# Performance work log

Hardware: AMD Instinct MI355X
Metric: run time of the kernel (lower is better)

The kernel has to match this reference:

```python
import jax, jax.numpy as jnp
import numpy as np

N_CLASSES = 16384
M = 2
D = 128


def setup_inputs() -> dict:
    key = jax.random.key(0)
    k1, k2 = jax.random.split(key)
    x = jax.random.normal(k1, (N_CLASSES * M, D), dtype=jnp.float32)
    anchor_idx = jax.random.randint(k2, (N_CLASSES,), 0, M, dtype=jnp.int64 if jax.config.jax_enable_x64 else jnp.int32).astype(jnp.int32)
    pos_idx = (1 - anchor_idx).astype(jnp.int32)  # randperm(2) -> positive is the other sample
    return {"x": x, "anchor_idx": anchor_idx, "pos_idx": pos_idx}


def reference(x, anchor_idx, pos_idx):
    # x: [N*M, D]; anchor_idx/pos_idx: [N] in [0, M)
    N = anchor_idx.shape[0]
    Dx = x.shape[1]
    xr = x.reshape(N, M, Dx)
    anchors = jnp.take_along_axis(xr, anchor_idx[:, None, None], axis=1)[:, 0, :]    # [N, D]
    positives = jnp.take_along_axis(xr, pos_idx[:, None, None], axis=1)[:, 0, :]     # [N, D]
    negs = xr[:, 1, :]                                                               # [N, D] (sample 1 of every class)
    # score[i, j] = a_i . (neg_j - pos_i) = a_i . neg_j - a_i . pos_i
    S = anchors @ negs.T                                                             # [N, N]
    ap = jnp.sum(anchors * positives, axis=1)                                        # [N]
    logits = S - ap[:, None]
    mask = ~jnp.eye(N, dtype=bool)                                                   # exclude j == i (own class)
    sums = jnp.sum(jnp.where(mask, jnp.exp(logits), jnp.float32(0.0)), axis=1)       # [N]
    return jnp.sum(jnp.log1p(sums))
```

## Files before the change

kernel.cpp:

```cpp
#include <hip/hip_runtime.h>
#include <hip/hip_bf16.h>
#include <math.h>

#define N_CLS 16384
#define DDIM  128
#define CSHIFT 50.0f
#define LDA 136

typedef __attribute__((ext_vector_type(8))) short short8;
typedef __attribute__((ext_vector_type(4))) float f32x4;

__device__ __forceinline__ unsigned short f2bf(float f) {
    __hip_bfloat16 h = __float2bfloat16(f);
    return *(unsigned short*)&h;
}

__global__ __launch_bounds__(256)
void prep_kernel(const float* __restrict__ x,
                 const int* __restrict__ aidx,
                 float* __restrict__ ap,
                 unsigned short* __restrict__ Abf,
                 unsigned short* __restrict__ Bfrag) {
    const int t = threadIdx.x;
    const int l = t & 31;
    const int i = blockIdx.x * 8 + (t >> 5);
    const float4 xa = *(const float4*)(x + (2L * i) * DDIM + l * 4);
    const float4 xb = *(const float4*)(x + (2L * i + 1) * DDIM + l * 4);
    const float4 av = (aidx[i] == 0) ? xa : xb;

    ushort4 a4; a4.x = f2bf(av.x); a4.y = f2bf(av.y); a4.z = f2bf(av.z); a4.w = f2bf(av.w);
    *(ushort4*)(Abf + (long)i * DDIM + l * 4) = a4;

    const int kc = l >> 3, q = (l >> 1) & 3, j0 = (l & 1) * 4;
    ushort4 b4; b4.x = f2bf(xb.x); b4.y = f2bf(xb.y); b4.z = f2bf(xb.z); b4.w = f2bf(xb.w);
    *(ushort4*)(Bfrag + ((long)((i >> 4) * 4 + kc)) * 512 + (q * 16 + (i & 15)) * 8 + j0) = b4;

    float d = xa.x * xb.x + xa.y * xb.y + xa.z * xb.z + xa.w * xb.w;
    d += __shfl_xor(d, 1, 64);
    d += __shfl_xor(d, 2, 64);
    d += __shfl_xor(d, 4, 64);
    d += __shfl_xor(d, 8, 64);
    d += __shfl_xor(d, 16, 64);
    if (l == 0) ap[i] = d;
}

__global__ __launch_bounds__(256)
void fused_kernel(const unsigned short* __restrict__ Abf,
                  const unsigned short* __restrict__ Bfrag,
                  float* __restrict__ partial) {
    __shared__ unsigned short As[128][LDA];

    const int tid = threadIdx.x;
    const int lane = tid & 63;
    const int w = tid >> 6;
    const int quad = lane >> 4;
    const int l15 = lane & 15;
    const int oct = blockIdx.x & 7;
    const int rt = blockIdx.x >> 3;
    const int rowBase = rt * 128;
    const int wm = (w >> 1) * 64;
    const int wh = w & 1;
    const int wn = wh * 64;

    {
        const int r = tid >> 1;
        const int half = (tid & 1) * 64;
        const uint4* ga = (const uint4*)(Abf + (long)(rowBase + r) * DDIM + half);
        uint4* la = (uint4*)&As[r][half];
        #pragma unroll
        for (int j = 0; j < 8; ++j) la[j] = ga[j];
    }
    __syncthreads();

    float rs[4][4];
    #pragma unroll
    for (int mt = 0; mt < 4; ++mt)
        #pragma unroll
        for (int reg = 0; reg < 4; ++reg) rs[mt][reg] = 0.0f;

    const unsigned short* bbase = Bfrag + ((long)(oct * 128 + wh * 4) * 4) * 512 + lane * 8;

    for (int it = 0; it < 16; ++it) {
        const int ct = oct * 16 + it;

        f32x4 acc[4][4];
        #pragma unroll
        for (int mt = 0; mt < 4; ++mt)
            #pragma unroll
            for (int nt = 0; nt < 4; ++nt) acc[mt][nt] = (f32x4){0.f, 0.f, 0.f, 0.f};

        #pragma unroll
        for (int kc = 0; kc < 4; ++kc) {
            short8 af[4], bfr[4];
            #pragma unroll
            for (int mt = 0; mt < 4; ++mt)
                af[mt] = *(const short8*)&As[wm + mt * 16 + l15][kc * 32 + quad * 8];
            #pragma unroll
            for (int nt = 0; nt < 4; ++nt)
                bfr[nt] = *(const short8*)(bbase + (long)it * 16384 + (nt * 4 + kc) * 512);
            #pragma unroll
            for (int mt = 0; mt < 4; ++mt)
                #pragma unroll
                for (int nt = 0; nt < 4; ++nt)
                    acc[mt][nt] = __builtin_amdgcn_mfma_f32_16x16x32_bf16(
                        af[mt], bfr[nt], acc[mt][nt], 0, 0, 0);
        }

        const int colBase = ct * 128 + wn;
        if (ct == rt) {
            #pragma unroll
            for (int mt = 0; mt < 4; ++mt)
                #pragma unroll
                for (int nt = 0; nt < 4; ++nt)
                    #pragma unroll
                    for (int reg = 0; reg < 4; ++reg) {
                        const int r = rowBase + wm + mt * 16 + quad * 4 + reg;
                        const int c = colBase + nt * 16 + l15;
                        const float e = __expf(acc[mt][nt][reg] - CSHIFT);
                        rs[mt][reg] += (r != c) ? e : 0.0f;
                    }
        } else {
            #pragma unroll
            for (int mt = 0; mt < 4; ++mt)
                #pragma unroll
                for (int nt = 0; nt < 4; ++nt)
                    #pragma unroll
                    for (int reg = 0; reg < 4; ++reg)
                        rs[mt][reg] += __expf(acc[mt][nt][reg] - CSHIFT);
        }
    }

    const int slot = oct * 2 + wh;
    #pragma unroll
    for (int mt = 0; mt < 4; ++mt)
        #pragma unroll
        for (int reg = 0; reg < 4; ++reg) {
            float v = rs[mt][reg];
            v += __shfl_xor(v, 1, 64);
            v += __shfl_xor(v, 2, 64);
            v += __shfl_xor(v, 4, 64);
            v += __shfl_xor(v, 8, 64);
            if (l15 == 0)
                partial[(long)slot * N_CLS + rowBase + wm + mt * 16 + quad * 4 + reg] = v;
        }
}

__global__ __launch_bounds__(256)
void finalize1_kernel(const float* __restrict__ partial,
                      const float* __restrict__ ap,
                      float* __restrict__ bsum) {
    __shared__ float red[256];
    const int t = threadIdx.x;
    const int row = blockIdx.x * 256 + t;
    float s = 0.0f;
    #pragma unroll
    for (int p = 0; p < 16; ++p) s += partial[(long)p * N_CLS + row];
    const float u = logf(s) + (CSHIFT - ap[row]);
    const float loss = (u > 25.0f) ? u : log1pf(__expf(u));
    red[t] = loss;
    __syncthreads();
    for (int st = 128; st > 0; st >>= 1) {
        if (t < st) red[t] += red[t + st];
        __syncthreads();
    }
    if (t == 0) bsum[blockIdx.x] = red[0];
}

__global__ __launch_bounds__(64)
void finalize2_kernel(const float* __restrict__ bsum, float* __restrict__ out) {
    float v = bsum[threadIdx.x];
    #pragma unroll
    for (int off = 32; off > 0; off >>= 1) v += __shfl_down(v, off, 64);
    if (threadIdx.x == 0) out[0] = v;
}

extern "C" void kernel_launch(void* const* d_in, const int* in_sizes, int n_in,
                              void* d_out, int out_size, void* d_ws, size_t ws_size,
                              hipStream_t stream) {
    const float* x    = (const float*)d_in[0];
    const int*   aidx = (const int*)d_in[1];

    char* ws = (char*)d_ws;
    float* ap            = (float*)(ws);
    float* bsum          = (float*)(ws + 65536);
    float* partial       = (float*)(ws + 131072);
    unsigned short* Abf  = (unsigned short*)(ws + 131072 + 1048576);
    unsigned short* Bfrag= (unsigned short*)(ws + 131072 + 1048576 + 4194304);

    prep_kernel<<<N_CLS / 8, 256, 0, stream>>>(x, aidx, ap, Abf, Bfrag);
    fused_kernel<<<1024, 256, 0, stream>>>(Abf, Bfrag, partial);
    finalize1_kernel<<<64, 256, 0, stream>>>(partial, ap, bsum);
    finalize2_kernel<<<1, 64, 0, stream>>>(bsum, (float*)d_out);
}
```

Measured before the change: 156.1 us.

## Keep A fragments in registers, double-buffer B loads, fold exp shift into MFMA

The prep kernel now writes A in the same MFMA fragment layout as B, pre-scaled by log2(e). The fused kernel then loads all A fragments into registers once, drops the LDS tile and the barrier, and ping-pongs B fragment loads so each k-chunk's global load overlaps the previous chunk's MFMAs. The exp shift is folded into the accumulator initial value so the epilogue uses raw exp2. The two finalize kernels are merged into one that uses an atomicAdd, with the output zeroed in prep. This costs more registers (launch bounds allow 2 blocks per CU) and adds bf16 rounding of the scaled A and a non-deterministic atomic summation order.

Result: faster. 142.7 us (-8.6%).

```diff
diff --git a/kernel.cpp b/kernel.cpp
--- a/kernel.cpp
+++ b/kernel.cpp
@@ -5,7 +5,14 @@
 #define N_CLS 16384
 #define DDIM  128
 #define CSHIFT 50.0f
-#define LDA 136
+#define LOG2E 1.4426950408889634f
+#define NEGC2 (-72.13475204444817f)
+
+#if __has_builtin(__builtin_amdgcn_exp2f)
+#define EXP2(x) __builtin_amdgcn_exp2f(x)
+#else
+#define EXP2(x) exp2f(x)
+#endif
 
 typedef __attribute__((ext_vector_type(8))) short short8;
 typedef __attribute__((ext_vector_type(4))) float f32x4;
@@ -19,8 +26,9 @@
 void prep_kernel(const float* __restrict__ x,
                  const int* __restrict__ aidx,
                  float* __restrict__ ap,
-                 unsigned short* __restrict__ Abf,
-                 unsigned short* __restrict__ Bfrag) {
+                 unsigned short* __restrict__ Afrag,
+                 unsigned short* __restrict__ Bfrag,
+                 float* __restrict__ out) {
     const int t = threadIdx.x;
     const int l = t & 31;
     const int i = blockIdx.x * 8 + (t >> 5);
@@ -28,12 +36,17 @@
     const float4 xb = *(const float4*)(x + (2L * i + 1) * DDIM + l * 4);
     const float4 av = (aidx[i] == 0) ? xa : xb;
 
-    ushort4 a4; a4.x = f2bf(av.x); a4.y = f2bf(av.y); a4.z = f2bf(av.z); a4.w = f2bf(av.w);
-    *(ushort4*)(Abf + (long)i * DDIM + l * 4) = a4;
-
     const int kc = l >> 3, q = (l >> 1) & 3, j0 = (l & 1) * 4;
-    ushort4 b4; b4.x = f2bf(xb.x); b4.y = f2bf(xb.y); b4.z = f2bf(xb.z); b4.w = f2bf(xb.w);
-    *(ushort4*)(Bfrag + ((long)((i >> 4) * 4 + kc)) * 512 + (q * 16 + (i & 15)) * 8 + j0) = b4;
+    const long base = ((long)((i >> 4) * 4 + kc)) * 512 + (q * 16 + (i & 15)) * 8 + j0;
+
+    ushort4 a4;
+    a4.x = f2bf(av.x * LOG2E); a4.y = f2bf(av.y * LOG2E);
+    a4.z = f2bf(av.z * LOG2E); a4.w = f2bf(av.w * LOG2E);
+    *(ushort4*)(Afrag + base) = a4;
+
+    ushort4 b4;
+    b4.x = f2bf(xb.x); b4.y = f2bf(xb.y); b4.z = f2bf(xb.z); b4.w = f2bf(xb.w);
+    *(ushort4*)(Bfrag + base) = b4;
 
     float d = xa.x * xb.x + xa.y * xb.y + xa.z * xb.z + xa.w * xb.w;
     d += __shfl_xor(d, 1, 64);
@@ -42,14 +55,13 @@
     d += __shfl_xor(d, 8, 64);
     d += __shfl_xor(d, 16, 64);
     if (l == 0) ap[i] = d;
-}
-
-__global__ __launch_bounds__(256)
-void fused_kernel(const unsigned short* __restrict__ Abf,
+    if (blockIdx.x == 0 && t == 0) out[0] = 0.0f;
+}
+
+__global__ __launch_bounds__(256, 2)
+void fused_kernel(const unsigned short* __restrict__ Afrag,
                   const unsigned short* __restrict__ Bfrag,
                   float* __restrict__ partial) {
-    __shared__ unsigned short As[128][LDA];
-
     const int tid = threadIdx.x;
     const int lane = tid & 63;
     const int w = tid >> 6;
@@ -57,56 +69,81 @@
     const int l15 = lane & 15;
     const int oct = blockIdx.x & 7;
     const int rt = blockIdx.x >> 3;
-    const int rowBase = rt * 128;
-    const int wm = (w >> 1) * 64;
+    const int wm2 = w >> 1;
     const int wh = w & 1;
-    const int wn = wh * 64;
-
+
+    short8 af[4][4];
     {
-        const int r = tid >> 1;
-        const int half = (tid & 1) * 64;
-        const uint4* ga = (const uint4*)(Abf + (long)(rowBase + r) * DDIM + half);
-        uint4* la = (uint4*)&As[r][half];
-        #pragma unroll
-        for (int j = 0; j < 8; ++j) la[j] = ga[j];
+        const unsigned short* abase =
+            Afrag + ((long)(rt * 8 + wm2 * 4) * 4) * 512 + lane * 8;
+        #pragma unroll
+        for (int mt = 0; mt < 4; ++mt)
+            #pragma unroll
+            for (int kc = 0; kc < 4; ++kc)
+                af[mt][kc] = *(const short8*)(abase + (mt * 4 + kc) * 512);
     }
-    __syncthreads();
-
-    float rs[4][4];
+
+    const unsigned short* bbase =
+        Bfrag + ((long)(oct * 128 + wh * 4) * 4) * 512 + lane * 8;
+
+    float rs[4][4] = {};
+    short8 bA[4], bB[4];
     #pragma unroll
-    for (int mt = 0; mt < 4; ++mt)
-        #pragma unroll
-        for (int reg = 0; reg < 4; ++reg) rs[mt][reg] = 0.0f;
-
-    const unsigned short* bbase = Bfrag + ((long)(oct * 128 + wh * 4) * 4) * 512 + lane * 8;
+    for (int nt = 0; nt < 4; ++nt)
+        bA[nt] = *(const short8*)(bbase + nt * 4 * 512);
 
     for (int it = 0; it < 16; ++it) {
+        const long itoff = (long)it * 16384;
+        const long nxoff = (it < 15) ? itoff + 16384 : itoff;
+
+        f32x4 acc[4][4];
+        #pragma unroll
+        for (int mt = 0; mt < 4; ++mt)
+            #pragma unroll
+            for (int nt = 0; nt < 4; ++nt)
+                acc[mt][nt] = (f32x4){NEGC2, NEGC2, NEGC2, NEGC2};
+
+        #pragma unroll
+        for (int nt = 0; nt < 4; ++nt)
+            bB[nt] = *(const short8*)(bbase + itoff + (nt * 4 + 1) * 512);
+        #pragma unroll
+        for (int mt = 0; mt < 4; ++mt)
+            #pragma unroll
+            for (int nt = 0; nt < 4; ++nt)
+                acc[mt][nt] = __builtin_amdgcn_mfma_f32_16x16x32_bf16(
+                    af[mt][0], bA[nt], acc[mt][nt], 0, 0, 0);
+
+        #pragma unroll
+        for (int nt = 0; nt < 4; ++nt)
+            bA[nt] = *(const short8*)(bbase + itoff + (nt * 4 + 2) * 512);
+        #pragma unroll
+        for (int mt = 0; mt < 4; ++mt)
+            #pragma unroll
+            for (int nt = 0; nt < 4; ++nt)
+                acc[mt][nt] = __builtin_amdgcn_mfma_f32_16x16x32_bf16(
+                    af[mt][1], bB[nt], acc[mt][nt], 0, 0, 0);
+
+        #pragma unroll
+        for (int nt = 0; nt < 4; ++nt)
+            bB[nt] = *(const short8*)(bbase + itoff + (nt * 4 + 3) * 512);
+        #pragma unroll
+        for (int mt = 0; mt < 4; ++mt)
+            #pragma unroll
+            for (int nt = 0; nt < 4; ++nt)
+                acc[mt][nt] = __builtin_amdgcn_mfma_f32_16x16x32_bf16(
+                    af[mt][2], bA[nt], acc[mt][nt], 0, 0, 0);
+
+        #pragma unroll
+        for (int nt = 0; nt < 4; ++nt)
+            bA[nt] = *(const short8*)(bbase + nxoff + nt * 4 * 512);
+        #pragma unroll
+        for (int mt = 0; mt < 4; ++mt)
+            #pragma unroll
+            for (int nt = 0; nt < 4; ++nt)
+                acc[mt][nt] = __builtin_amdgcn_mfma_f32_16x16x32_bf16(
+                    af[mt][3], bB[nt], acc[mt][nt], 0, 0, 0);
+
         const int ct = oct * 16 + it;
-
-        f32x4 acc[4][4];
-        #pragma unroll
-        for (int mt = 0; mt < 4; ++mt)
-            #pragma unroll
-            for (int nt = 0; nt < 4; ++nt) acc[mt][nt] = (f32x4){0.f, 0.f, 0.f, 0.f};
-
-        #pragma unroll
-        for (int kc = 0; kc < 4; ++kc) {
-            short8 af[4], bfr[4];
-            #pragma unroll
-            for (int mt = 0; mt < 4; ++mt)
-                af[mt] = *(const short8*)&As[wm + mt * 16 + l15][kc * 32 + quad * 8];
-            #pragma unroll
-            for (int nt = 0; nt < 4; ++nt)
-                bfr[nt] = *(const short8*)(bbase + (long)it * 16384 + (nt * 4 + kc) * 512);
-            #pragma unroll
-            for (int mt = 0; mt < 4; ++mt)
-                #pragma unroll
-                for (int nt = 0; nt < 4; ++nt)
-                    acc[mt][nt] = __builtin_amdgcn_mfma_f32_16x16x32_bf16(
-                        af[mt], bfr[nt], acc[mt][nt], 0, 0, 0);
-        }
-
-        const int colBase = ct * 128 + wn;
         if (ct == rt) {
             #pragma unroll
             for (int mt = 0; mt < 4; ++mt)
@@ -114,10 +151,10 @@
                 for (int nt = 0; nt < 4; ++nt)
                     #pragma unroll
                     for (int reg = 0; reg < 4; ++reg) {
-                        const int r = rowBase + wm + mt * 16 + quad * 4 + reg;
-                        const int c = colBase + nt * 16 + l15;
-                        const float e = __expf(acc[mt][nt][reg] - CSHIFT);
-                        rs[mt][reg] += (r != c) ? e : 0.0f;
+                        const bool diag = (wm2 == wh) && (mt == nt) &&
+                                          (quad * 4 + reg == l15);
+                        const float e = EXP2(acc[mt][nt][reg]);
+                        rs[mt][reg] += diag ? 0.0f : e;
                     }
         } else {
             #pragma unroll
@@ -126,11 +163,12 @@
                 for (int nt = 0; nt < 4; ++nt)
                     #pragma unroll
                     for (int reg = 0; reg < 4; ++reg)
-                        rs[mt][reg] += __expf(acc[mt][nt][reg] - CSHIFT);
+                        rs[mt][reg] += EXP2(acc[mt][nt][reg]);
         }
     }
 
     const int slot = oct * 2 + wh;
+    const int rowBase = rt * 128 + wm2 * 64;
     #pragma unroll
     for (int mt = 0; mt < 4; ++mt)
         #pragma unroll
@@ -141,14 +179,14 @@
             v += __shfl_xor(v, 4, 64);
             v += __shfl_xor(v, 8, 64);
             if (l15 == 0)
-                partial[(long)slot * N_CLS + rowBase + wm + mt * 16 + quad * 4 + reg] = v;
+                partial[(long)slot * N_CLS + rowBase + mt * 16 + quad * 4 + reg] = v;
         }
 }
 
 __global__ __launch_bounds__(256)
-void finalize1_kernel(const float* __restrict__ partial,
-                      const float* __restrict__ ap,
-                      float* __restrict__ bsum) {
+void finalize_kernel(const float* __restrict__ partial,
+                     const float* __restrict__ ap,
+                     float* __restrict__ out) {
     __shared__ float red[256];
     const int t = threadIdx.x;
     const int row = blockIdx.x * 256 + t;
@@ -163,15 +201,7 @@
         if (t < st) red[t] += red[t + st];
         __syncthreads();
     }
-    if (t == 0) bsum[blockIdx.x] = red[0];
-}
-
-__global__ __launch_bounds__(64)
-void finalize2_kernel(const float* __restrict__ bsum, float* __restrict__ out) {
-    float v = bsum[threadIdx.x];
-    #pragma unroll
-    for (int off = 32; off > 0; off >>= 1) v += __shfl_down(v, off, 64);
-    if (threadIdx.x == 0) out[0] = v;
+    if (t == 0) atomicAdd(out, red[0]);
 }
 
 extern "C" void kernel_launch(void* const* d_in, const int* in_sizes, int n_in,
@@ -181,14 +211,12 @@
     const int*   aidx = (const int*)d_in[1];
 
     char* ws = (char*)d_ws;
-    float* ap            = (float*)(ws);
-    float* bsum          = (float*)(ws + 65536);
-    float* partial       = (float*)(ws + 131072);
-    unsigned short* Abf  = (unsigned short*)(ws + 131072 + 1048576);
-    unsigned short* Bfrag= (unsigned short*)(ws + 131072 + 1048576 + 4194304);
-
-    prep_kernel<<<N_CLS / 8, 256, 0, stream>>>(x, aidx, ap, Abf, Bfrag);
-    fused_kernel<<<1024, 256, 0, stream>>>(Abf, Bfrag, partial);
-    finalize1_kernel<<<64, 256, 0, stream>>>(partial, ap, bsum);
-    finalize2_kernel<<<1, 64, 0, stream>>>(bsum, (float*)d_out);
-}
+    float* ap             = (float*)(ws);
+    float* partial        = (float*)(ws + 131072);
+    unsigned short* Afrag = (unsigned short*)(ws + 131072 + 1048576);
+    unsigned short* Bfrag = (unsigned short*)(ws + 131072 + 1048576 + 4194304);
+
+    prep_kernel<<<N_CLS / 8, 256, 0, stream>>>(x, aidx, ap, Afrag, Bfrag, (float*)d_out);
+    fused_kernel<<<1024, 256, 0, stream>>>(Afrag, Bfrag, partial);
+    finalize_kernel<<<64, 256, 0, stream>>>(partial, ap, (float*)d_out);
+}
```
